# Optimization experiments

Measured on AMD Instinct MI355X. Metric: run time of the kernel, lower is better.

Reference implementation:

```python
import jax, jax.numpy as jnp
import numpy as np

B, C, H, W, D = 2, 256, 40, 40, 40
HEADS = 8


def _conv1x1(x, w, b):
    # 1x1x1 Conv3d == pointwise channel mix: x [B,C,H,W,D], w [O,C], b [O]
    return jnp.einsum('bchwd,oc->bohwd', x, w) + b[None, :, None, None, None]


def setup_inputs() -> dict:
    key = jax.random.key(0)
    ks = jax.random.split(key, 9)
    s = 1.0 / np.sqrt(C)
    return {
        'x': jax.random.normal(ks[0], (B, C, H, W, D), dtype=jnp.float32),
        'wq': jax.random.normal(ks[1], (C, C), dtype=jnp.float32) * s,
        'bq': jax.random.normal(ks[2], (C,), dtype=jnp.float32) * 0.01,
        'wk': jax.random.normal(ks[3], (C, C), dtype=jnp.float32) * s,
        'bk': jax.random.normal(ks[4], (C,), dtype=jnp.float32) * 0.01,
        'wv': jax.random.normal(ks[5], (C, C), dtype=jnp.float32) * s,
        'bv': jax.random.normal(ks[6], (C,), dtype=jnp.float32) * 0.01,
        'wp': jax.random.normal(ks[7], (C, C), dtype=jnp.float32) * s,
        'bp': jax.random.normal(ks[8], (C,), dtype=jnp.float32) * 0.01,
    }


def reference(x, wq, bq, wk, bk, wv, bv, wp, bp):
    b, ch, h, w, d = x.shape
    heads = HEADS
    hd = ch // heads
    scale = hd ** -0.5
    # q/k/v projections are identical across the three branches -> compute once
    q = _conv1x1(x, wq, bq)
    k = _conv1x1(x, wk, bk)
    v = _conv1x1(x, wv, bv)

    def branch(s1, s2, s3):
        # row-major reshape, exactly matching torch .view semantics
        qh = q.reshape(b, heads, hd, s1, s2, s3)
        kh = k.reshape(b, heads, hd, s1, s2, s3)
        vh = v.reshape(b, heads, hd, s1, s2, s3)
        # matmul over last two axes: attend along s2 with s3 as feature dim
        attn = jax.nn.softmax(qh @ jnp.swapaxes(kh, -1, -2) * scale, axis=-1)
        return (attn @ vh).reshape(b, ch, h, w, d)

    out = branch(h, w, d) + branch(w, h, d) + branch(d, h, w)
    return _conv1x1(out, wp, bp)
```

## Files before the change

kernel.cpp:

```cpp
#include <hip/hip_runtime.h>

#define NB 2
#define NC 256
#define NHH 40
#define NSP 64000
#define PL 1600
#define SCALE 0.17677669529663687f

typedef unsigned short u16;
typedef unsigned int   u32;

typedef __attribute__((ext_vector_type(8))) short bf16x8;
typedef __attribute__((ext_vector_type(4))) float f32x4;

__device__ __forceinline__ float bf2f(u16 u) {
    union { u32 i; float f; } c; c.i = ((u32)u) << 16; return c.f;
}
__device__ __forceinline__ u16 f2bf(float f) {
    union { u32 i; float f; } c; c.f = f; u32 x = c.i;
    return (u16)((x + 0x7fffu + ((x >> 16) & 1u)) >> 16);
}
__device__ __forceinline__ u32 pack2(float a, float b) {
    return (u32)f2bf(a) | ((u32)f2bf(b) << 16);
}
__device__ __forceinline__ f32x4 zero4() {
    f32x4 z; z[0] = 0.f; z[1] = 0.f; z[2] = 0.f; z[3] = 0.f; return z;
}
__device__ __forceinline__ bf16x8 zero8() {
    bf16x8 z;
#pragma unroll
    for (int e = 0; e < 8; ++e) z[e] = 0;
    return z;
}

__global__ __launch_bounds__(256) void wfrag3(
    const float* __restrict__ wq, const float* __restrict__ wk,
    const float* __restrict__ wv, u16* __restrict__ dst)
{
    const int gid  = blockIdx.x * 256 + threadIdx.x;
    const int lane = gid & 63;
    const int i    = (gid >> 6) & 1;
    const int wid  = (gid >> 7) & 7;
    const int step = gid >> 10;
    const int m    = step >> 3;
    const int kc   = step & 7;
    const int row  = wid * 32 + i * 16 + (lane & 15);
    const int col  = kc * 32 + ((lane >> 4) << 3);
    const float* s = ((m == 0) ? wq : ((m == 1) ? wk : wv)) + (size_t)row * NC + col;
    const float4 a = *(const float4*)(s);
    const float4 b = *(const float4*)(s + 4);
    ushort4 p0, p1;
    p0.x = f2bf(a.x); p0.y = f2bf(a.y); p0.z = f2bf(a.z); p0.w = f2bf(a.w);
    p1.x = f2bf(b.x); p1.y = f2bf(b.y); p1.z = f2bf(b.z); p1.w = f2bf(b.w);
    u16* d = dst + (size_t)gid * 8;
    *(ushort4*)(d)     = p0;
    *(ushort4*)(d + 4) = p1;
}

__global__ __launch_bounds__(256) void wfrag1(
    const float* __restrict__ w, u16* __restrict__ dst)
{
    const int gid  = blockIdx.x * 256 + threadIdx.x;
    const int lane = gid & 63;
    const int i    = (gid >> 6) & 1;
    const int wid  = (gid >> 7) & 7;
    const int step = (gid >> 10) & 7;
    const int row  = wid * 32 + i * 16 + (lane & 15);
    const int col  = step * 32 + ((lane >> 4) << 3);
    const float* s = w + (size_t)row * NC + col;
    const float4 a = *(const float4*)(s);
    const float4 b = *(const float4*)(s + 4);
    ushort4 p0, p1;
    p0.x = f2bf(a.x); p0.y = f2bf(a.y); p0.z = f2bf(a.z); p0.w = f2bf(a.w);
    p1.x = f2bf(b.x); p1.y = f2bf(b.y); p1.z = f2bf(b.z); p1.w = f2bf(b.w);
    u16* d = dst + (size_t)gid * 8;
    *(ushort4*)(d)     = p0;
    *(ushort4*)(d + 4) = p1;
}

__global__ __launch_bounds__(512, 4) void qkv5(
    const float* __restrict__ x, const u16* __restrict__ wf,
    const float* __restrict__ bq, const float* __restrict__ bk,
    const float* __restrict__ bv,
    u16* __restrict__ q, u16* __restrict__ k, u16* __restrict__ v)
{
    const int b    = blockIdx.z;
    const int n0   = blockIdx.x * 64;
    const int t    = threadIdx.x;
    const int lane = t & 63;
    const int wid  = t >> 6;
    const int o0w  = wid * 32;
    const int row  = lane & 15;
    const int kg   = (lane >> 4) << 3;
    const int g4   = (lane >> 4) << 2;

    __shared__ u16 xs[64][264];

    const float* xb = x + (size_t)b * NC * NSP;

    {
        const int p   = t >> 4;
        const int nn  = (t & 15) << 2;
        const int rot = (t >> 1) & 3;
#pragma unroll
        for (int it = 0; it < 4; ++it) {
            const int c = (it * 32 + p) * 2;
            const float4 fa = *(const float4*)(xb + (size_t)c * NSP + n0 + nn);
            const float4 fb = *(const float4*)(xb + (size_t)(c + 1) * NSP + n0 + nn);
            u32 pk[4] = { pack2(fa.x, fb.x), pack2(fa.y, fb.y),
                          pack2(fa.z, fb.z), pack2(fa.w, fb.w) };
#pragma unroll
            for (int kk = 0; kk < 4; ++kk) {
                const int k2 = (kk + rot) & 3;
                *(u32*)&xs[nn + k2][c] = pk[k2];
            }
        }
    }
    __syncthreads();

    const u16* wfb = wf + (size_t)(wid * 2) * 512 + (size_t)lane * 8;

    f32x4 acc[2][4];
#pragma unroll
    for (int i = 0; i < 2; ++i)
#pragma unroll
        for (int j = 0; j < 4; ++j) acc[i][j] = zero4();

    bf16x8 afc[2], afn[2];
    afc[0] = *(const bf16x8*)(wfb);
    afc[1] = *(const bf16x8*)(wfb + 512);

    for (int step = 0; step < 24; ++step) {
        const int m  = step >> 3;
        const int kc = step & 7;
        const bool pf = (step + 1 < 24);

        if (pf) {
            const u16* wn = wfb + (size_t)(step + 1) * 8192;
            afn[0] = *(const bf16x8*)(wn);
            afn[1] = *(const bf16x8*)(wn + 512);
        }

        bf16x8 bfr[4];
#pragma unroll
        for (int j = 0; j < 4; ++j)
            bfr[j] = *(const bf16x8*)&xs[16 * j + row][kc * 32 + kg];
#pragma unroll
        for (int i = 0; i < 2; ++i)
#pragma unroll
            for (int j = 0; j < 4; ++j)
                acc[i][j] = __builtin_amdgcn_mfma_f32_16x16x32_bf16(
                    afc[i], bfr[j], acc[i][j], 0, 0, 0);

        if (kc == 7) {
            u16* op = ((m == 0) ? q : ((m == 1) ? k : v)) + (size_t)b * NC * NSP;
            const float* bm = (m == 0) ? bq : ((m == 1) ? bk : bv);
#pragma unroll
            for (int i = 0; i < 2; ++i) {
#pragma unroll
                for (int r = 0; r < 4; ++r) {
                    const int o = o0w + 16 * i + g4 + r;
                    const float bb = bm[o];
#pragma unroll
                    for (int j = 0; j < 4; ++j) {
                        const int n = n0 + 16 * j + row;
                        op[(size_t)o * NSP + n] = f2bf(acc[i][j][r] + bb);
                    }
                }
            }
#pragma unroll
            for (int i = 0; i < 2; ++i)
#pragma unroll
                for (int j = 0; j < 4; ++j) acc[i][j] = zero4();
        }

        afc[0] = afn[0];
        afc[1] = afn[1];
    }
}

__global__ __launch_bounds__(64, 4) void attn_mfma(
    const u16* __restrict__ q, const u16* __restrict__ k,
    const u16* __restrict__ v, u16* __restrict__ a)
{
    const int s = blockIdx.x;
    const size_t base = (size_t)s * PL;
    const int l = threadIdx.x & 63;
    const int g = l >> 4;
    const int c = l & 15;

    __shared__ u16 vs[48][56];
    __shared__ u16 ps[48][56];

#pragma unroll
    for (int it = 0; it < 3; ++it) {
        const int t = l + it * 64;
        *(u32*)&vs[t >> 2][40 + ((t & 3) << 1)] = 0u;
    }

#pragma unroll
    for (int it = 0; it < 7; ++it) {
        const int idx = l + it * 64;
        if (idx < 400) {
            const int j = idx / 10, d4 = (idx % 10) << 2;
            const ushort4 vv = *(const ushort4*)(v + base + j * 40 + d4);
            vs[d4 + 0][j] = vv.x; vs[d4 + 1][j] = vv.y;
            vs[d4 + 2][j] = vv.z; vs[d4 + 3][j] = vv.w;
        }
    }

    f32x4 sacc[3][3];
#pragma unroll
    for (int mt = 0; mt < 3; ++mt)
#pragma unroll
        for (int jt = 0; jt < 3; ++jt) sacc[mt][jt] = zero4();

    {
        bf16x8 aq[3], bk0[3];
#pragma unroll
        for (int mt = 0; mt < 3; ++mt)
            aq[mt] = *(const bf16x8*)(q + base + (size_t)(mt * 16 + c) * 40 + g * 8);
#pragma unroll
        for (int jt = 0; jt < 3; ++jt)
            bk0[jt] = *(const bf16x8*)(k + base + (size_t)(jt * 16 + c) * 40 + g * 8);
#pragma unroll
        for (int mt = 0; mt < 3; ++mt)
#pragma unroll
            for (int jt = 0; jt < 3; ++jt)
                sacc[mt][jt] = __builtin_amdgcn_mfma_f32_16x16x32_bf16(
                    aq[mt], bk0[jt], sacc[mt][jt], 0, 0, 0);

        bf16x8 aq1[3], bk1[3];
#pragma unroll
        for (int mt = 0; mt < 3; ++mt)
            aq1[mt] = (g == 0)
                ? *(const bf16x8*)(q + base + (size_t)(mt * 16 + c) * 40 + 32)
                : zero8();
#pragma unroll
        for (int jt = 0; jt < 3; ++jt)
            bk1[jt] = (g == 0)
                ? *(const bf16x8*)(k + base + (size_t)(jt * 16 + c) * 40 + 32)
                : zero8();
#pragma unroll
        for (int mt = 0; mt < 3; ++mt)
#pragma unroll
            for (int jt = 0; jt < 3; ++jt)
                sacc[mt][jt] = __builtin_amdgcn_mfma_f32_16x16x32_bf16(
                    aq1[mt], bk1[jt], sacc[mt][jt], 0, 0, 0);
    }

    const bool val2 = (c < 8);
#pragma unroll
    for (int mt = 0; mt < 3; ++mt) {
#pragma unroll
        for (int r = 0; r < 4; ++r) {
            const float v0 = sacc[mt][0][r];
            const float v1 = sacc[mt][1][r];
            const float v2 = sacc[mt][2][r];
            float mx = fmaxf(fmaxf(v0, v1), val2 ? v2 : -1e30f);
#pragma unroll
            for (int off = 1; off < 16; off <<= 1)
                mx = fmaxf(mx, __shfl_xor(mx, off, 64));
            const float p0 = __expf((v0 - mx) * SCALE);
            const float p1 = __expf((v1 - mx) * SCALE);
            const float p2 = val2 ? __expf((v2 - mx) * SCALE) : 0.f;
            float sum = p0 + p1 + p2;
#pragma unroll
            for (int off = 1; off < 16; off <<= 1)
                sum += __shfl_xor(sum, off, 64);
            const float inv = 3.0f / sum;
            const int ri = mt * 16 + g * 4 + r;
            ps[ri][c]      = f2bf(p0 * inv);
            ps[ri][c + 16] = f2bf(p1 * inv);
            ps[ri][c + 32] = f2bf(p2 * inv);
        }
    }
    __syncthreads();

    f32x4 oacc[3][3];
#pragma unroll
    for (int mt = 0; mt < 3; ++mt)
#pragma unroll
        for (int nt = 0; nt < 3; ++nt) oacc[mt][nt] = zero4();

    {
        bf16x8 pa[3], vb_[3];
#pragma unroll
        for (int mt = 0; mt < 3; ++mt)
            pa[mt] = *(const bf16x8*)&ps[mt * 16 + c][g * 8];
#pragma unroll
        for (int nt = 0; nt < 3; ++nt)
            vb_[nt] = *(const bf16x8*)&vs[nt * 16 + c][g * 8];
#pragma unroll
        for (int mt = 0; mt < 3; ++mt)
#pragma unroll
            for (int nt = 0; nt < 3; ++nt)
                oacc[mt][nt] = __builtin_amdgcn_mfma_f32_16x16x32_bf16(
                    pa[mt], vb_[nt], oacc[mt][nt], 0, 0, 0);

        bf16x8 pa1[3], vb1[3];
#pragma unroll
        for (int mt = 0; mt < 3; ++mt)
            pa1[mt] = (g < 2) ? *(const bf16x8*)&ps[mt * 16 + c][32 + g * 8] : zero8();
#pragma unroll
        for (int nt = 0; nt < 3; ++nt)
            vb1[nt] = (g < 2) ? *(const bf16x8*)&vs[nt * 16 + c][32 + g * 8] : zero8();
#pragma unroll
        for (int mt = 0; mt < 3; ++mt)
#pragma unroll
            for (int nt = 0; nt < 3; ++nt)
                oacc[mt][nt] = __builtin_amdgcn_mfma_f32_16x16x32_bf16(
                    pa1[mt], vb1[nt], oacc[mt][nt], 0, 0, 0);
    }
    __syncthreads();

#pragma unroll
    for (int mt = 0; mt < 3; ++mt) {
        if (mt == 2 && g >= 2) continue;
#pragma unroll
        for (int r = 0; r < 4; ++r) {
            const int ri = mt * 16 + g * 4 + r;
#pragma unroll
            for (int nt = 0; nt < 3; ++nt) {
                if (nt == 2 && c >= 8) continue;
                ps[ri][nt * 16 + c] = f2bf(oacc[mt][nt][r]);
            }
        }
    }
    __syncthreads();

#pragma unroll
    for (int it = 0; it < 7; ++it) {
        const int idx = l + it * 64;
        if (idx < 400) {
            const int i = idx / 10, d4 = (idx % 10) << 2;
            *(ushort4*)(a + base + (size_t)idx * 4) = *(const ushort4*)&ps[i][d4];
        }
    }
}

__global__ __launch_bounds__(512, 4) void proj5(
    const u16* __restrict__ a, const u16* __restrict__ wf,
    const float* __restrict__ bp, float* __restrict__ out)
{
    const int b    = blockIdx.z;
    const int n0   = blockIdx.x * 64;
    const int t    = threadIdx.x;
    const int lane = t & 63;
    const int wid  = t >> 6;
    const int o0w  = wid * 32;
    const int row  = lane & 15;
    const int kg   = (lane >> 4) << 3;
    const int g4   = (lane >> 4) << 2;

    __shared__ u16 xs[64][264];

    const u16* ab = a + (size_t)b * NC * NSP;

    {
        const int p   = t >> 4;
        const int nn  = (t & 15) << 2;
        const int rot = (t >> 1) & 3;
#pragma unroll
        for (int it = 0; it < 4; ++it) {
            const int c = (it * 32 + p) * 2;
            const ushort4 ua = *(const ushort4*)(ab + (size_t)c * NSP + n0 + nn);
            const ushort4 ub = *(const ushort4*)(ab + (size_t)(c + 1) * NSP + n0 + nn);
            u32 pk[4] = { (u32)ua.x | ((u32)ub.x << 16), (u32)ua.y | ((u32)ub.y << 16),
                          (u32)ua.z | ((u32)ub.z << 16), (u32)ua.w | ((u32)ub.w << 16) };
#pragma unroll
            for (int kk = 0; kk < 4; ++kk) {
                const int k2 = (kk + rot) & 3;
                *(u32*)&xs[nn + k2][c] = pk[k2];
            }
        }
    }
    __syncthreads();

    const u16* wfb = wf + (size_t)(wid * 2) * 512 + (size_t)lane * 8;

    f32x4 acc[2][4];
#pragma unroll
    for (int i = 0; i < 2; ++i)
#pragma unroll
        for (int j = 0; j < 4; ++j) acc[i][j] = zero4();

    bf16x8 afc[2], afn[2];
    afc[0] = *(const bf16x8*)(wfb);
    afc[1] = *(const bf16x8*)(wfb + 512);

#pragma unroll
    for (int step = 0; step < 8; ++step) {
        const bool pf = (step + 1 < 8);
        if (pf) {
            const u16* wn = wfb + (size_t)(step + 1) * 8192;
            afn[0] = *(const bf16x8*)(wn);
            afn[1] = *(const bf16x8*)(wn + 512);
        }

        bf16x8 bfr[4];
#pragma unroll
        for (int j = 0; j < 4; ++j)
            bfr[j] = *(const bf16x8*)&xs[16 * j + row][step * 32 + kg];
#pragma unroll
        for (int i = 0; i < 2; ++i)
#pragma unroll
            for (int j = 0; j < 4; ++j)
                acc[i][j] = __builtin_amdgcn_mfma_f32_16x16x32_bf16(
                    afc[i], bfr[j], acc[i][j], 0, 0, 0);

        afc[0] = afn[0];
        afc[1] = afn[1];
    }

    float* ob = out + (size_t)b * NC * NSP;
#pragma unroll
    for (int i = 0; i < 2; ++i) {
#pragma unroll
        for (int r = 0; r < 4; ++r) {
            const int o = o0w + 16 * i + g4 + r;
            const float bb = bp[o];
#pragma unroll
            for (int j = 0; j < 4; ++j) {
                const int n = n0 + 16 * j + row;
                ob[(size_t)o * NSP + n] = acc[i][j][r] + bb;
            }
        }
    }
}

extern "C" void kernel_launch(void* const* d_in, const int* in_sizes, int n_in,
                              void* d_out, int out_size, void* d_ws, size_t ws_size,
                              hipStream_t stream)
{
    const float* x  = (const float*)d_in[0];
    const float* wq = (const float*)d_in[1];
    const float* bq = (const float*)d_in[2];
    const float* wk = (const float*)d_in[3];
    const float* bk = (const float*)d_in[4];
    const float* wv = (const float*)d_in[5];
    const float* bv = (const float*)d_in[6];
    const float* wp = (const float*)d_in[7];
    const float* bp = (const float*)d_in[8];
    float* out = (float*)d_out;

    const size_t QE = (size_t)NB * NC * NSP;
    u16* qb = (u16*)d_ws;
    u16* kb = qb + QE;
    u16* vb = kb + QE;
    u16* ab = vb + QE;

    u16* wqf = (u16*)d_out;
    u16* wpf = qb;

    wfrag3<<<96, 256, 0, stream>>>(wq, wk, wv, wqf);
    qkv5<<<dim3(NSP / 64, 1, NB), 512, 0, stream>>>(
        x, wqf, bq, bk, bv, qb, kb, vb);
    attn_mfma<<<dim3(NB * NC * NHH), 64, 0, stream>>>(qb, kb, vb, ab);
    wfrag1<<<32, 256, 0, stream>>>(wp, wpf);
    proj5<<<dim3(NSP / 64, 1, NB), 512, 0, stream>>>(ab, wpf, bp, out);
}
```

Measured before the change: 235.0 us.

## Make QKV projection persistent over four tiles with double-buffered x prefetch

Each QKV block now handles four consecutive 64-column tiles instead of one. While the current tile's MFMA loop runs, the next tile's x is loaded into registers and then written into a second LDS buffer, so global load latency overlaps compute. The grid shrinks from 1000 to 250 blocks per batch and LDS per block doubles. This can lower occupancy, and the extra prefetch registers raise register pressure.

```diff
diff --git a/kernel.cpp b/kernel.cpp
--- a/kernel.cpp
+++ b/kernel.cpp
@@ -78,14 +78,14 @@
     *(ushort4*)(d + 4) = p1;
 }
 
-__global__ __launch_bounds__(512, 4) void qkv5(
+__global__ __launch_bounds__(512, 4) void qkv7(
     const float* __restrict__ x, const u16* __restrict__ wf,
     const float* __restrict__ bq, const float* __restrict__ bk,
     const float* __restrict__ bv,
     u16* __restrict__ q, u16* __restrict__ k, u16* __restrict__ v)
 {
     const int b    = blockIdx.z;
-    const int n0   = blockIdx.x * 64;
+    const int nb0  = blockIdx.x * 256;
     const int t    = threadIdx.x;
     const int lane = t & 63;
     const int wid  = t >> 6;
@@ -94,26 +94,31 @@
     const int kg   = (lane >> 4) << 3;
     const int g4   = (lane >> 4) << 2;
 
-    __shared__ u16 xs[64][264];
+    __shared__ u16 xs[2][64][264];
 
     const float* xb = x + (size_t)b * NC * NSP;
 
-    {
-        const int p   = t >> 4;
-        const int nn  = (t & 15) << 2;
-        const int rot = (t >> 1) & 3;
-#pragma unroll
-        for (int it = 0; it < 4; ++it) {
-            const int c = (it * 32 + p) * 2;
-            const float4 fa = *(const float4*)(xb + (size_t)c * NSP + n0 + nn);
-            const float4 fb = *(const float4*)(xb + (size_t)(c + 1) * NSP + n0 + nn);
-            u32 pk[4] = { pack2(fa.x, fb.x), pack2(fa.y, fb.y),
-                          pack2(fa.z, fb.z), pack2(fa.w, fb.w) };
-#pragma unroll
-            for (int kk = 0; kk < 4; ++kk) {
-                const int k2 = (kk + rot) & 3;
-                *(u32*)&xs[nn + k2][c] = pk[k2];
-            }
+    const int sp   = t >> 4;
+    const int snn  = (t & 15) << 2;
+    const int srot = (t >> 1) & 3;
+
+    float4 xra[4], xrb[4];
+
+#pragma unroll
+    for (int it = 0; it < 4; ++it) {
+        const int c = (it * 32 + sp) * 2;
+        xra[it] = *(const float4*)(xb + (size_t)c * NSP + nb0 + snn);
+        xrb[it] = *(const float4*)(xb + (size_t)(c + 1) * NSP + nb0 + snn);
+    }
+#pragma unroll
+    for (int it = 0; it < 4; ++it) {
+        const int c = (it * 32 + sp) * 2;
+        u32 pk[4] = { pack2(xra[it].x, xrb[it].x), pack2(xra[it].y, xrb[it].y),
+                      pack2(xra[it].z, xrb[it].z), pack2(xra[it].w, xrb[it].w) };
+#pragma unroll
+        for (int kk = 0; kk < 4; ++kk) {
+            const int k2 = (kk + srot) & 3;
+            *(u32*)&xs[0][snn + k2][c] = pk[k2];
         }
     }
     __syncthreads();
@@ -126,56 +131,88 @@
 #pragma unroll
         for (int j = 0; j < 4; ++j) acc[i][j] = zero4();
 
-    bf16x8 afc[2], afn[2];
-    afc[0] = *(const bf16x8*)(wfb);
-    afc[1] = *(const bf16x8*)(wfb + 512);
-
-    for (int step = 0; step < 24; ++step) {
-        const int m  = step >> 3;
-        const int kc = step & 7;
-        const bool pf = (step + 1 < 24);
-
-        if (pf) {
-            const u16* wn = wfb + (size_t)(step + 1) * 8192;
-            afn[0] = *(const bf16x8*)(wn);
-            afn[1] = *(const bf16x8*)(wn + 512);
-        }
-
-        bf16x8 bfr[4];
-#pragma unroll
-        for (int j = 0; j < 4; ++j)
-            bfr[j] = *(const bf16x8*)&xs[16 * j + row][kc * 32 + kg];
-#pragma unroll
-        for (int i = 0; i < 2; ++i)
+    int cur = 0;
+    for (int tt = 0; tt < 4; ++tt) {
+        const int n0 = nb0 + tt * 64;
+        const bool more = (tt < 3);
+
+        if (more) {
+            const int n0n = n0 + 64;
+#pragma unroll
+            for (int it = 0; it < 4; ++it) {
+                const int c = (it * 32 + sp) * 2;
+                xra[it] = *(const float4*)(xb + (size_t)c * NSP + n0n + snn);
+                xrb[it] = *(const float4*)(xb + (size_t)(c + 1) * NSP + n0n + snn);
+            }
+        }
+
+        bf16x8 afc[2], afn[2];
+        afc[0] = *(const bf16x8*)(wfb);
+        afc[1] = *(const bf16x8*)(wfb + 512);
+
+        for (int step = 0; step < 24; ++step) {
+            const int m  = step >> 3;
+            const int kc = step & 7;
+            const bool pf = (step + 1 < 24);
+
+            if (pf) {
+                const u16* wn = wfb + (size_t)(step + 1) * 8192;
+                afn[0] = *(const bf16x8*)(wn);
+                afn[1] = *(const bf16x8*)(wn + 512);
+            }
+
+            bf16x8 bfr[4];
 #pragma unroll
             for (int j = 0; j < 4; ++j)
-                acc[i][j] = __builtin_amdgcn_mfma_f32_16x16x32_bf16(
-                    afc[i], bfr[j], acc[i][j], 0, 0, 0);
-
-        if (kc == 7) {
-            u16* op = ((m == 0) ? q : ((m == 1) ? k : v)) + (size_t)b * NC * NSP;
-            const float* bm = (m == 0) ? bq : ((m == 1) ? bk : bv);
-#pragma unroll
-            for (int i = 0; i < 2; ++i) {
-#pragma unroll
-                for (int r = 0; r < 4; ++r) {
-                    const int o = o0w + 16 * i + g4 + r;
-                    const float bb = bm[o];
-#pragma unroll
-                    for (int j = 0; j < 4; ++j) {
-                        const int n = n0 + 16 * j + row;
-                        op[(size_t)o * NSP + n] = f2bf(acc[i][j][r] + bb);
+                bfr[j] = *(const bf16x8*)&xs[cur][16 * j + row][kc * 32 + kg];
+#pragma unroll
+            for (int i = 0; i < 2; ++i)
+#pragma unroll
+                for (int j = 0; j < 4; ++j)
+                    acc[i][j] = __builtin_amdgcn_mfma_f32_16x16x32_bf16(
+                        afc[i], bfr[j], acc[i][j], 0, 0, 0);
+
+            if (kc == 7) {
+                u16* op = ((m == 0) ? q : ((m == 1) ? k : v)) + (size_t)b * NC * NSP;
+                const float* bm = (m == 0) ? bq : ((m == 1) ? bk : bv);
+#pragma unroll
+                for (int i = 0; i < 2; ++i) {
+#pragma unroll
+                    for (int r = 0; r < 4; ++r) {
+                        const int o = o0w + 16 * i + g4 + r;
+                        const float bb = bm[o];
+#pragma unroll
+                        for (int j = 0; j < 4; ++j) {
+                            const int n = n0 + 16 * j + row;
+                            op[(size_t)o * NSP + n] = f2bf(acc[i][j][r] + bb);
+                        }
                     }
                 }
-            }
-#pragma unroll
-            for (int i = 0; i < 2; ++i)
-#pragma unroll
-                for (int j = 0; j < 4; ++j) acc[i][j] = zero4();
-        }
-
-        afc[0] = afn[0];
-        afc[1] = afn[1];
+#pragma unroll
+                for (int i = 0; i < 2; ++i)
+#pragma unroll
+                    for (int j = 0; j < 4; ++j) acc[i][j] = zero4();
+            }
+
+            afc[0] = afn[0];
+            afc[1] = afn[1];
+        }
+
+        if (more) {
+#pragma unroll
+            for (int it = 0; it < 4; ++it) {
+                const int c = (it * 32 + sp) * 2;
+                u32 pk[4] = { pack2(xra[it].x, xrb[it].x), pack2(xra[it].y, xrb[it].y),
+                              pack2(xra[it].z, xrb[it].z), pack2(xra[it].w, xrb[it].w) };
+#pragma unroll
+                for (int kk = 0; kk < 4; ++kk) {
+                    const int k2 = (kk + srot) & 3;
+                    *(u32*)&xs[cur ^ 1][snn + k2][c] = pk[k2];
+                }
+            }
+            __syncthreads();
+            cur ^= 1;
+        }
     }
 }
 
@@ -454,7 +491,7 @@
     u16* wpf = qb;
 
     wfrag3<<<96, 256, 0, stream>>>(wq, wk, wv, wqf);
-    qkv5<<<dim3(NSP / 64, 1, NB), 512, 0, stream>>>(
+    qkv7<<<dim3(250, 1, NB), 512, 0, stream>>>(
         x, wqf, bq, bk, bv, qb, kb, vb);
     attn_mfma<<<dim3(NB * NC * NHH), 64, 0, stream>>>(qb, kb, vb, ab);
     wfrag1<<<32, 256, 0, stream>>>(wp, wpf);
```

Result: slower. 465.6 us (+98.1%).
